# Optimization experiments

Measured on AMD Instinct MI355X. Metric: run time of the kernel, lower is better.

Reference implementation:

```python
import jax, jax.numpy as jnp
import numpy as np

B, S, HID = 2, 2048, 1024
H, KV, D = 8, 4, 128
GROUPS = H // KV
SCALE = D ** -0.5
ROPE_THETA = 10000.0


def _rope_tables(seq_len, dim):
    inv = 1.0 / (ROPE_THETA ** (jnp.arange(0, dim, 2, dtype=jnp.float32) / dim))
    t = jnp.arange(seq_len, dtype=jnp.float32)
    freqs = jnp.outer(t, inv)                          # [S, D/2]
    emb = jnp.concatenate([freqs, freqs], axis=-1)     # [S, D]
    return jnp.cos(emb), jnp.sin(emb)


def _rotate_half(x):
    x1, x2 = jnp.split(x, 2, axis=-1)
    return jnp.concatenate([-x2, x1], axis=-1)


def setup_inputs() -> dict:
    key = jax.random.key(0)
    ks = jax.random.split(key, 7)
    std = 0.02
    hidden = jax.random.normal(ks[0], (B, S, HID), jnp.float32)
    Wq = jax.random.normal(ks[1], (HID, H * D), jnp.float32) * std
    Wk = jax.random.normal(ks[2], (HID, KV * D), jnp.float32) * std
    Wv = jax.random.normal(ks[3], (HID, KV * D), jnp.float32) * std
    Wdt = jax.random.normal(ks[4], (KV * D, H), jnp.float32) * std
    A = jax.random.normal(ks[5], (H,), jnp.float32) * 0.1
    Wo = jax.random.normal(ks[6], (H * D, HID), jnp.float32) * std
    cos, sin = _rope_tables(S, D)
    causal_mask = jnp.triu(jnp.ones((S, S), jnp.int32), 1)[None, None]  # 1 = masked
    return dict(hidden=hidden, Wq=Wq, Wk=Wk, Wv=Wv, Wdt=Wdt, A=A, Wo=Wo,
                cos=cos, sin=sin, causal_mask=causal_mask)


def reference(hidden, Wq, Wk, Wv, Wdt, A, Wo, cos, sin, causal_mask):
    # q/k/v projections -> [B, heads, S, D]
    q = (hidden @ Wq).reshape(B, S, H, D).transpose(0, 2, 1, 3)
    k = (hidden @ Wk).reshape(B, S, KV, D).transpose(0, 2, 1, 3)
    v = (hidden @ Wv).reshape(B, S, KV, D).transpose(0, 2, 1, 3)
    # RoPE
    c = cos[None, None]  # [1,1,S,D]
    s = sin[None, None]
    q = q * c + _rotate_half(q) * s
    k = k * c + _rotate_half(k) * s
    # dynamic mask: dt_proj over flattened per-position value states
    v_flat = v.transpose(0, 2, 1, 3).reshape(B, S, KV * D)
    dt = v_flat @ Wdt                                        # [B, S, H]
    dyn = jnp.exp(A[None, None, :] * jax.nn.softplus(dt))    # [B, S, H]
    attn_bias = dyn.transpose(0, 2, 1)[:, :, None, :]        # [B, H, 1, kv]
    min_val = jnp.finfo(jnp.float32).min
    attn_bias = jnp.where(causal_mask != 0, min_val, attn_bias)  # [B, H, S, S]
    # GQA repeat of kv heads
    k_rep = jnp.repeat(k, GROUPS, axis=1)
    v_rep = jnp.repeat(v, GROUPS, axis=1)
    scores = jnp.einsum('bhqd,bhkd->bhqk', q, k_rep) * SCALE + attn_bias
    w = jax.nn.softmax(scores.astype(jnp.float32), axis=-1).astype(hidden.dtype)
    out = jnp.einsum('bhqk,bhkd->bhqd', w, v_rep)
    out = out.transpose(0, 2, 1, 3).reshape(B, S, H * D)
    return out @ Wo
```

## Files before the change

kernel.cpp:

```cpp
#include <hip/hip_runtime.h>

typedef unsigned short u16;
typedef unsigned int   u32;
typedef __bf16 bf16;
typedef bf16  bf16x8 __attribute__((ext_vector_type(8)));
typedef float f32x4  __attribute__((ext_vector_type(4)));

#define S_LEN 2048
#define SCALE 0.08838834764831845f
#define SMAX  8.0f

__device__ __forceinline__ float bf2f(u16 u) {
  union { u32 i; float f; } v; v.i = ((u32)u) << 16; return v.f;
}
__device__ __forceinline__ u16 f2b(float f) {
  union { float f; u32 i; } v; v.f = f;
  u32 x = v.i;
  u32 r = x + 0x7fffu + ((x >> 16) & 1u);
  return (u16)(r >> 16);
}
__device__ __forceinline__ float2 bfpair(u32 u) {
  union { u32 i; float f; } lo, hi;
  lo.i = u << 16; hi.i = u & 0xffff0000u;
  float2 r; r.x = lo.f; r.y = hi.f; return r;
}

__device__ __forceinline__ void gl_lds16(const u16* g, u16* l) {
  __builtin_amdgcn_global_load_lds(
      (const __attribute__((address_space(1))) void*)g,
      (__attribute__((address_space(3))) void*)l, 16, 0, 0);
}

__device__ __forceinline__ void load16(const float* p, u16* dst) {
  #pragma unroll
  for (int i = 0; i < 16; i += 4) {
    float4 v = *(const float4*)(p + i);
    dst[i]     = f2b(v.x); dst[i + 1] = f2b(v.y);
    dst[i + 2] = f2b(v.z); dst[i + 3] = f2b(v.w);
  }
}

__device__ __forceinline__ void storeo(float* p, float v) { *p = v; }
__device__ __forceinline__ void storeo(u16* p, float v)   { *p = f2b(v); }

__device__ __forceinline__ bf16x8 frag8(const u16* p) {
  union { uint4 u; bf16x8 v; } c;
  c.u = *(const uint4*)p;
  return c.v;
}
__device__ __forceinline__ f32x4 zero4() {
  f32x4 z = {0.f, 0.f, 0.f, 0.f}; return z;
}

__global__ __launch_bounds__(256) void prep_kernel(
    const float* __restrict__ H, u16* __restrict__ HB,
    const float* __restrict__ Wq, const float* __restrict__ Wk,
    const float* __restrict__ Wv, const float* __restrict__ Wo,
    u16* __restrict__ Wqt, u16* __restrict__ Wkt,
    u16* __restrict__ Wvt, u16* __restrict__ Wot)
{
  const int bid = blockIdx.x;
  if (bid < 2048) {
    const size_t base = ((size_t)bid * 256 + threadIdx.x) * 8;
    float4 a = *(const float4*)(H + base);
    float4 b = *(const float4*)(H + base + 4);
    u16 tmp[8];
    tmp[0]=f2b(a.x); tmp[1]=f2b(a.y); tmp[2]=f2b(a.z); tmp[3]=f2b(a.w);
    tmp[4]=f2b(b.x); tmp[5]=f2b(b.y); tmp[6]=f2b(b.z); tmp[7]=f2b(b.w);
    *(uint4*)(HB + base) = *(uint4*)tmp;
    return;
  }
  const int b2 = bid - 2048;
  const float* src; u16* dst; int N, ko, no;
  if (b2 < 256)      { src = Wq; dst = Wqt; N = 1024; int q = b2;       ko = (q >> 4) * 64; no = (q & 15) * 64; }
  else if (b2 < 384) { src = Wk; dst = Wkt; N = 512;  int q = b2 - 256; ko = (q >> 3) * 64; no = (q & 7) * 64; }
  else if (b2 < 512) { src = Wv; dst = Wvt; N = 512;  int q = b2 - 384; ko = (q >> 3) * 64; no = (q & 7) * 64; }
  else               { src = Wo; dst = Wot; N = 1024; int q = b2 - 512; ko = (q >> 4) * 64; no = (q & 15) * 64; }

  __shared__ __align__(16) u16 T[64][68];
  const int t = threadIdx.x;
  const int r = t >> 2, c = (t & 3) * 16;
  {
    u16 tmp[16];
    load16(src + (size_t)(ko + r) * N + no + c, tmp);
    *(uint4*)&T[r][c]     = *(uint4*)tmp;
    *(uint4*)&T[r][c + 8] = *(uint4*)(tmp + 8);
  }
  __syncthreads();
  {
    u16 tmp[16];
    #pragma unroll
    for (int j = 0; j < 16; ++j) tmp[j] = T[c + j][r];
    u16* o = dst + (size_t)(no + r) * 1024 + ko + c;
    *(uint4*)o       = *(uint4*)tmp;
    *(uint4*)(o + 8) = *(uint4*)(tmp + 8);
  }
}

__global__ __launch_bounds__(512) void gemm3(
    const u16* __restrict__ A, int lda, int Kdim,
    const u16* __restrict__ W0, u16* __restrict__ O0, int ldo0,
    const u16* __restrict__ W1, u16* __restrict__ O1, int ldo1,
    const u16* __restrict__ W2, u16* __restrict__ O2, int ldo2,
    int c1, int c2,
    const float* __restrict__ cosb, const float* __restrict__ sinb, int ropeLim,
    u16* __restrict__ VTg)
{
  const int flat = blockIdx.y * gridDim.x + blockIdx.x;
  const int xcd = flat & 7, rr = flat >> 3;
  const int bx = ((xcd & 1) << 3) + (rr & 7);
  const int by = ((xcd >> 1) << 3) + (rr >> 3);
  const int n0 = bx * 128;
  const int m0 = by * 128;
  const u16* W; u16* O; int ldo, col;
  if (n0 < c1)      { W = W0; O = O0; ldo = ldo0; col = n0; }
  else if (n0 < c2) { W = W1; O = O1; ldo = ldo1; col = n0 - c1; }
  else              { W = W2; O = O2; ldo = ldo2; col = n0 - c2; }
  const bool doRope = (n0 < ropeLim);
  const bool isV    = (n0 >= c2);

  __shared__ __align__(16) u16 As[2][128 * 64];
  __shared__ __align__(16) u16 Bs[2][128 * 64];

  const int t    = threadIdx.x;
  const int w    = t >> 6, lane = t & 63, quad = lane >> 4, l16 = lane & 15;
  const int sw   = l16 & 7;
  const int srow = lane >> 3;
  const int schk = (lane & 7) ^ srow;
  int kcs[2];
  #pragma unroll
  for (int ks = 0; ks < 2; ++ks) kcs[ks] = ((ks * 4 + quad) ^ sw) * 8;

  const u16* Ag = A + (size_t)(m0 + w * 16 + srow) * lda + schk * 8;
  const u16* Bg = W + (size_t)(col + w * 16 + srow) * Kdim + schk * 8;

  f32x4 acc[8];
  #pragma unroll
  for (int nt = 0; nt < 8; ++nt) acc[nt] = zero4();

  #pragma unroll
  for (int j = 0; j < 2; ++j) {
    gl_lds16(Ag + (size_t)(j * 8) * lda, &As[0][(w * 2 + j) * 512]);
    gl_lds16(Bg + (size_t)(j * 8) * Kdim, &Bs[0][(w * 2 + j) * 512]);
  }

  int cur = 0;
  for (int k0 = 0; k0 < Kdim; k0 += 64, cur ^= 1) {
    __syncthreads();
    if (k0 + 64 < Kdim) {
      #pragma unroll
      for (int j = 0; j < 2; ++j) {
        gl_lds16(Ag + (size_t)(j * 8) * lda + k0 + 64, &As[cur ^ 1][(w * 2 + j) * 512]);
        gl_lds16(Bg + (size_t)(j * 8) * Kdim + k0 + 64, &Bs[cur ^ 1][(w * 2 + j) * 512]);
      }
    }
    #pragma unroll
    for (int ks = 0; ks < 2; ++ks) {
      bf16x8 a0 = frag8(&As[cur][(w * 16 + l16) * 64 + kcs[ks]]);
      #pragma unroll
      for (int nt = 0; nt < 8; ++nt) {
        bf16x8 bw = frag8(&Bs[cur][(nt * 16 + l16) * 64 + kcs[ks]]);
        acc[nt] = __builtin_amdgcn_mfma_f32_16x16x32_bf16(a0, bw, acc[nt], 0, 0, 0);
      }
    }
  }

  if (doRope) {
    #pragma unroll
    for (int r = 0; r < 4; ++r) {
      const int m = m0 + w * 16 + quad * 4 + r;
      const int sp_ = m & (S_LEN - 1);
      const float* cp = cosb + (size_t)sp_ * 128;
      const float* sp = sinb + (size_t)sp_ * 128;
      #pragma unroll
      for (int nt = 0; nt < 4; ++nt) {
        const int d = nt * 16 + l16;
        const float a  = acc[nt][r];
        const float bb = acc[nt + 4][r];
        acc[nt][r]     = a * cp[d]       - bb * sp[d];
        acc[nt + 4][r] = bb * cp[d + 64] + a * sp[d + 64];
      }
    }
  }

  #pragma unroll
  for (int nt = 0; nt < 8; ++nt)
    #pragma unroll
    for (int r = 0; r < 4; ++r) {
      const int m = m0 + w * 16 + quad * 4 + r;
      const int n = col + nt * 16 + l16;
      O[(size_t)m * ldo + n] = f2b(acc[nt][r]);
    }

  if (isV) {
    #pragma unroll
    for (int nt = 0; nt < 8; ++nt) {
      const int m = m0 + w * 16 + quad * 4;
      const int bb_ = m >> 11, ss = m & (S_LEN - 1);
      const int d = col + nt * 16 + l16;
      u16 tmp4[4];
      #pragma unroll
      for (int r = 0; r < 4; ++r) tmp4[r] = f2b(acc[nt][r]);
      u16* dst = VTg + ((size_t)((bb_ * 4 + (d >> 7)) * 128 + (d & 127))) * S_LEN + ss;
      *(uint2*)dst = *(const uint2*)tmp4;
    }
  }
}

template <typename TO>
__global__ __launch_bounds__(512) void gemm2(
    const u16* __restrict__ A, int lda, int Kdim,
    const u16* __restrict__ W0, TO* __restrict__ O0, int ldo0,
    const u16* __restrict__ W1, TO* __restrict__ O1, int ldo1,
    const u16* __restrict__ W2, TO* __restrict__ O2, int ldo2,
    int c1, int c2)
{
  const int flat = blockIdx.y * gridDim.x + blockIdx.x;
  const int xcd = flat & 7, rr = flat >> 3;
  const int bx = ((xcd & 1) << 3) + (rr & 7);
  const int by = ((xcd >> 1) << 3) + (rr >> 3);
  const int n0 = bx * 64;
  const int m0 = by * 128;
  const u16* W; TO* O; int ldo, col;
  if (n0 < c1)      { W = W0; O = O0; ldo = ldo0; col = n0; }
  else if (n0 < c2) { W = W1; O = O1; ldo = ldo1; col = n0 - c1; }
  else              { W = W2; O = O2; ldo = ldo2; col = n0 - c2; }

  __shared__ __align__(16) u16 As[2][128 * 64];
  __shared__ __align__(16) u16 Bs[2][64 * 64];

  const int t    = threadIdx.x;
  const int w    = t >> 6, lane = t & 63, quad = lane >> 4, l16 = lane & 15;
  const int sw   = l16 & 7;
  const int srow = lane >> 3;
  const int schk = (lane & 7) ^ srow;
  int kcs[2];
  #pragma unroll
  for (int ks = 0; ks < 2; ++ks) kcs[ks] = ((ks * 4 + quad) ^ sw) * 8;

  const u16* Ag = A + (size_t)(m0 + w * 16 + srow) * lda + schk * 8;
  const u16* Bg = W + (size_t)(col + w * 8 + srow) * Kdim + schk * 8;

  f32x4 acc[4];
  #pragma unroll
  for (int nt = 0; nt < 4; ++nt) acc[nt] = zero4();

  #pragma unroll
  for (int j = 0; j < 2; ++j)
    gl_lds16(Ag + (size_t)(j * 8) * lda, &As[0][(w * 2 + j) * 512]);
  gl_lds16(Bg, &Bs[0][w * 512]);

  int cur = 0;
  for (int k0 = 0; k0 < Kdim; k0 += 64, cur ^= 1) {
    __syncthreads();
    if (k0 + 64 < Kdim) {
      #pragma unroll
      for (int j = 0; j < 2; ++j)
        gl_lds16(Ag + (size_t)(j * 8) * lda + k0 + 64, &As[cur ^ 1][(w * 2 + j) * 512]);
      gl_lds16(Bg + (size_t)k0 + 64, &Bs[cur ^ 1][w * 512]);
    }
    #pragma unroll
    for (int ks = 0; ks < 2; ++ks) {
      bf16x8 a0 = frag8(&As[cur][(w * 16 + l16) * 64 + kcs[ks]]);
      #pragma unroll
      for (int nt = 0; nt < 4; ++nt) {
        bf16x8 bw = frag8(&Bs[cur][(nt * 16 + l16) * 64 + kcs[ks]]);
        acc[nt] = __builtin_amdgcn_mfma_f32_16x16x32_bf16(a0, bw, acc[nt], 0, 0, 0);
      }
    }
  }
  #pragma unroll
  for (int nt = 0; nt < 4; ++nt)
    #pragma unroll
    for (int r = 0; r < 4; ++r) {
      const int m = m0 + w * 16 + quad * 4 + r;
      const int n = col + nt * 16 + l16;
      storeo(O + (size_t)m * ldo + n, acc[nt][r]);
    }
}

__global__ __launch_bounds__(256) void dyn_kernel(const u16* __restrict__ Vb, const float* __restrict__ Wdt,
                                                  const float* __restrict__ Af, float* __restrict__ dynT)
{
  __shared__ __align__(16) float Wl[4096];
  const int t = threadIdx.x;
  #pragma unroll
  for (int i = 0; i < 4; ++i)
    *(float4*)&Wl[(t + i * 256) * 4] = *(const float4*)(Wdt + (t + i * 256) * 4);
  __syncthreads();

  const int wid = t >> 6, lane = t & 63;
  const int pos = blockIdx.x * 4 + wid;
  float acc[8];
  #pragma unroll
  for (int h = 0; h < 8; ++h) acc[h] = 0.f;
  for (int j = lane; j < 512; j += 64) {
    float v = bf2f(Vb[(size_t)pos * 512 + j]);
    float4 w0 = *(const float4*)&Wl[j * 8];
    float4 w1 = *(const float4*)&Wl[j * 8 + 4];
    acc[0] += v * w0.x; acc[1] += v * w0.y; acc[2] += v * w0.z; acc[3] += v * w0.w;
    acc[4] += v * w1.x; acc[5] += v * w1.y; acc[6] += v * w1.z; acc[7] += v * w1.w;
  }
  #pragma unroll
  for (int off = 32; off > 0; off >>= 1)
    #pragma unroll
    for (int h = 0; h < 8; ++h) acc[h] += __shfl_down(acc[h], off, 64);
  if (lane == 0) {
    const int b = pos >> 11, s = pos & (S_LEN - 1);
    #pragma unroll
    for (int h = 0; h < 8; ++h) {
      float dt = acc[h];
      float sp = (dt > 20.f) ? dt : log1pf(__expf(dt));
      dynT[(size_t)(b * 8 + h) * S_LEN + s] = __expf(Af[h] * sp);
    }
  }
}

__global__ __launch_bounds__(256, 2) void attn_mfma(const u16* __restrict__ Qb, const u16* __restrict__ Kb,
                                                    const u16* __restrict__ VTg, const float* __restrict__ dynT,
                                                    u16* __restrict__ ctx,
                                                    u16* __restrict__ PO, float* __restrict__ PL)
{
  const int idx = blockIdx.x;
  const int g = (idx & 7) | (((idx >> 3) & 1) << 3);
  const int b = g >> 3, h = g & 7, kvh = h >> 1;
  const int f = idx >> 4;
  int s, c, kt0, kt1;
  if (f < 16)      { s = 16 + f; c = 0; kt0 = 0; kt1 = 7; }
  else if (f < 32) { s = 47 - f; c = 1; kt0 = 8; kt1 = s >> 1; }
  else             { s = 47 - f; c = 0; kt0 = 0; kt1 = s >> 1; }
  const int q0 = s * 64;
  const int dt = s >> 1;

  __shared__ __align__(16) u16 Ks[128 * 128];
  __shared__ __align__(16) u16 Vs[128 * 128];
  __shared__ __align__(16) u16 Ps[4][16 * 128];

  const int t = threadIdx.x;
  const int wid = t >> 6, lane = t & 63, quad = lane >> 4, l16 = lane & 15;
  const int sw = l16 & 7, hi = l16 >> 3;

  int kcs[4];
  #pragma unroll
  for (int ks = 0; ks < 4; ++ks) kcs[ks] = ((ks * 4 + quad) ^ sw) * 8;

  const u16* KgL[2];
  const u16* VgL[2];
  {
    const int g0 = hi * 8 + (sw ^ quad);
    const int g1 = hi * 8 + (sw ^ quad ^ 4);
    KgL[0] = Kb + (size_t)(b * S_LEN + wid * 32 + quad) * 512 + kvh * 128 + g0 * 8;
    KgL[1] = Kb + (size_t)(b * S_LEN + wid * 32 + 4 + quad) * 512 + kvh * 128 + g1 * 8;
    VgL[0] = VTg + ((size_t)((b * 4 + kvh) * 128 + wid * 32 + quad)) * S_LEN + g0 * 8;
    VgL[1] = VTg + ((size_t)((b * 4 + kvh) * 128 + wid * 32 + 4 + quad)) * S_LEN + g1 * 8;
  }

  bf16x8 qf[4];
  {
    const u16* qrow = Qb + (size_t)(b * S_LEN + q0 + wid * 16 + l16) * 1024 + h * 128 + quad * 8;
    #pragma unroll
    for (int ks = 0; ks < 4; ++ks) qf[ks] = frag8(qrow + ks * 32);
  }

  const float* dynbase = dynT + (size_t)(b * 8 + h) * S_LEN + l16;

  f32x4 accO[8];
  #pragma unroll
  for (int nt = 0; nt < 8; ++nt) accO[nt] = zero4();
  float l_lane[4] = {0.f, 0.f, 0.f, 0.f};

  for (int kt = kt0; kt <= kt1; ++kt) {
    const int k0 = kt * 128;
    __syncthreads();
    #pragma unroll
    for (int j = 0; j < 8; ++j)
      gl_lds16(KgL[j & 1] + (size_t)(k0 + (j >> 1) * 8) * 512, &Ks[(wid * 8 + j) * 512]);
    #pragma unroll
    for (int j = 0; j < 8; ++j)
      gl_lds16(VgL[j & 1] + (size_t)((j >> 1) * 8) * S_LEN + k0, &Vs[(wid * 8 + j) * 512]);
    float dv[8];
    #pragma unroll
    for (int nt = 0; nt < 8; ++nt) dv[nt] = dynbase[k0 + nt * 16];
    __syncthreads();

    f32x4 accS[8];
    #pragma unroll
    for (int nt = 0; nt < 8; ++nt) accS[nt] = zero4();
    __builtin_amdgcn_s_setprio(1);
    #pragma unroll
    for (int ks = 0; ks < 4; ++ks)
      #pragma unroll
      for (int nt = 0; nt < 8; ++nt)
        accS[nt] = __builtin_amdgcn_mfma_f32_16x16x32_bf16(
            qf[ks], frag8(&Ks[(nt * 16 + l16) * 128 + kcs[ks]]), accS[nt], 0, 0, 0);
    __builtin_amdgcn_s_setprio(0);

    if (kt < dt) {
      #pragma unroll
      for (int nt = 0; nt < 8; ++nt)
        #pragma unroll
        for (int r = 0; r < 4; ++r) {
          float p = __expf(fmaf(accS[nt][r], SCALE, dv[nt]) - SMAX);
          l_lane[r] += p;
          const int prow = quad * 4 + r;
          Ps[wid][prow * 128 + (((nt * 2 + hi) ^ (prow & 7)) << 3) + sw] = f2b(p);
        }
    } else {
      const int qq = (s & 1) * 64 + wid * 16 + quad * 4;
      #pragma unroll
      for (int nt = 0; nt < 8; ++nt) {
        const int kk = nt * 16 + l16;
        #pragma unroll
        for (int r = 0; r < 4; ++r) {
          float p = (kk > qq + r) ? 0.f
                    : __expf(fmaf(accS[nt][r], SCALE, dv[nt]) - SMAX);
          l_lane[r] += p;
          const int prow = quad * 4 + r;
          Ps[wid][prow * 128 + (((nt * 2 + hi) ^ (prow & 7)) << 3) + sw] = f2b(p);
        }
      }
    }

    __builtin_amdgcn_s_setprio(1);
    #pragma unroll
    for (int ks = 0; ks < 4; ++ks) {
      bf16x8 a = frag8(&Ps[wid][l16 * 128 + kcs[ks]]);
      #pragma unroll
      for (int nt = 0; nt < 8; ++nt)
        accO[nt] = __builtin_amdgcn_mfma_f32_16x16x32_bf16(
            a, frag8(&Vs[(nt * 16 + l16) * 128 + kcs[ks]]), accO[nt], 0, 0, 0);
    }
    __builtin_amdgcn_s_setprio(0);
  }

  #pragma unroll
  for (int off = 1; off < 16; off <<= 1)
    #pragma unroll
    for (int r = 0; r < 4; ++r) l_lane[r] += __shfl_xor(l_lane[r], off, 64);

  if (s < 16) {
    float linv[4];
    #pragma unroll
    for (int r = 0; r < 4; ++r) linv[r] = 1.f / l_lane[r];
    #pragma unroll
    for (int nt = 0; nt < 8; ++nt)
      #pragma unroll
      for (int r = 0; r < 4; ++r) {
        const int qq = q0 + wid * 16 + quad * 4 + r;
        const int d  = nt * 16 + l16;
        ctx[(size_t)(b * S_LEN + qq) * 1024 + h * 128 + d] = f2b(accO[nt][r] * linv[r]);
      }
  } else {
    const int slot = g * 32 + (s - 16) * 2 + c;
    u16 tmp[32];
    #pragma unroll
    for (int nt = 0; nt < 8; ++nt)
      #pragma unroll
      for (int r = 0; r < 4; ++r) tmp[nt * 4 + r] = f2b(accO[nt][r]);
    u16* po = PO + (size_t)slot * 8192 + wid * 2048 + lane * 32;
    #pragma unroll
    for (int i = 0; i < 4; ++i) *(uint4*)(po + i * 8) = *(uint4*)(tmp + i * 8);
    if (l16 == 0) {
      #pragma unroll
      for (int r = 0; r < 4; ++r) PL[slot * 64 + wid * 16 + quad * 4 + r] = l_lane[r];
    }
  }
}

__global__ __launch_bounds__(256) void attn_combine(const u16* __restrict__ PO, const float* __restrict__ PL,
                                                    u16* __restrict__ ctx)
{
  const int sx = (int)blockIdx.x;
  const int s = 16 + sx;
  const int g = (int)blockIdx.y;
  const int b = g >> 3, h = g & 7;
  const int slot0 = g * 32 + sx * 2;
  const int t = threadIdx.x;
  const int wid = t >> 6, lane = t & 63, quad = lane >> 4, l16 = lane & 15;

  float acc[32];
  #pragma unroll
  for (int i = 0; i < 32; ++i) acc[i] = 0.f;
  float ls[4] = {0.f, 0.f, 0.f, 0.f};

  #pragma unroll
  for (int cth = 0; cth < 2; ++cth) {
    const u16* po = PO + (size_t)(slot0 + cth) * 8192 + wid * 2048 + lane * 32;
    #pragma unroll
    for (int i = 0; i < 4; ++i) {
      uint4 v = *(const uint4*)(po + i * 8);
      u32 u[4] = {v.x, v.y, v.z, v.w};
      #pragma unroll
      for (int j = 0; j < 4; ++j) {
        float2 p = bfpair(u[j]);
        acc[i * 8 + 2 * j]     += p.x;
        acc[i * 8 + 2 * j + 1] += p.y;
      }
    }
    #pragma unroll
    for (int r = 0; r < 4; ++r) ls[r] += PL[(slot0 + cth) * 64 + wid * 16 + quad * 4 + r];
  }

  float linv[4];
  #pragma unroll
  for (int r = 0; r < 4; ++r) linv[r] = 1.f / ls[r];
  #pragma unroll
  for (int nt = 0; nt < 8; ++nt)
    #pragma unroll
    for (int r = 0; r < 4; ++r) {
      const int qq = s * 64 + wid * 16 + quad * 4 + r;
      const int d  = nt * 16 + l16;
      ctx[(size_t)(b * S_LEN + qq) * 1024 + h * 128 + d] = f2b(acc[nt * 4 + r] * linv[r]);
    }
}

extern "C" void kernel_launch(void* const* d_in, const int* in_sizes, int n_in,
                              void* d_out, int out_size, void* d_ws, size_t ws_size,
                              hipStream_t stream)
{
  const float* hidden = (const float*)d_in[0];
  const float* Wq     = (const float*)d_in[1];
  const float* Wk     = (const float*)d_in[2];
  const float* Wv     = (const float*)d_in[3];
  const float* Wdt    = (const float*)d_in[4];
  const float* Af     = (const float*)d_in[5];
  const float* Wo     = (const float*)d_in[6];
  const float* cosb   = (const float*)d_in[7];
  const float* sinb   = (const float*)d_in[8];
  float* out = (float*)d_out;

  u16* Qb  = (u16*)d_ws;
  u16* Kb  = Qb + (size_t)4096 * 1024;
  u16* Vb  = Kb + (size_t)4096 * 512;
  u16* VTg = Vb + (size_t)4096 * 512;
  float* dynT = (float*)(VTg + (size_t)4096 * 512);
  u16* PO = (u16*)(dynT + (size_t)16 * S_LEN);
  float* PL = (float*)(PO + (size_t)16 * 32 * 8192);
  u16* HB  = (u16*)(PL + (size_t)16 * 32 * 64);
  u16* Wqt = HB  + (size_t)4096 * 1024;
  u16* Wkt = Wqt + (size_t)1024 * 1024;
  u16* Wvt = Wkt + (size_t)512 * 1024;
  u16* Wot = Wvt + (size_t)512 * 1024;
  u16* ctx = Qb;

  prep_kernel<<<2816, 256, 0, stream>>>(hidden, HB, Wq, Wk, Wv, Wo, Wqt, Wkt, Wvt, Wot);
  gemm3<<<dim3(16, 32), 512, 0, stream>>>(HB, 1024, 1024,
      Wqt, Qb, 1024,
      Wkt, Kb,  512,
      Wvt, Vb,  512,
      1024, 1536,
      cosb, sinb, 1536, VTg);
  dyn_kernel<<<1024, 256, 0, stream>>>(Vb, Wdt, Af, dynT);
  attn_mfma<<<768, 256, 0, stream>>>(Qb, Kb, VTg, dynT, ctx, PO, PL);
  attn_combine<<<dim3(16, 16), 256, 0, stream>>>(PO, PL, ctx);
  gemm2<float><<<dim3(16, 32), 512, 0, stream>>>(ctx, 1024, 1024,
      Wot, out, 1024,
      Wot, out, 1024,
      Wot, out, 1024,
      1 << 30, 1 << 30);
}
```

Measured before the change: 196.1 us.

## Enlarge attention query tile to 128 rows with 8-wave blocks

The attention kernel now processes 128 query rows per block using 8 waves (512 threads) instead of 64 rows with 4 waves. Each K/V tile loaded into LDS is shared by twice as many query rows, which halves global K/V traffic per query. The causal split schedule and combine kernel are remapped to 128-row tiles with half as many blocks and partial slots. In exchange, there are fewer blocks in flight, the causal diagonal work is coarser, and larger LDS use per block may lower occupancy.

```diff
diff --git a/kernel.cpp b/kernel.cpp
--- a/kernel.cpp
+++ b/kernel.cpp
@@ -316,25 +316,27 @@
   }
 }
 
-__global__ __launch_bounds__(256, 2) void attn_mfma(const u16* __restrict__ Qb, const u16* __restrict__ Kb,
-                                                    const u16* __restrict__ VTg, const float* __restrict__ dynT,
-                                                    u16* __restrict__ ctx,
-                                                    u16* __restrict__ PO, float* __restrict__ PL)
+__global__ __launch_bounds__(512) void attn_mfma(const u16* __restrict__ Qb, const u16* __restrict__ Kb,
+                                                 const u16* __restrict__ VTg, const float* __restrict__ dynT,
+                                                 u16* __restrict__ ctx,
+                                                 u16* __restrict__ PO, float* __restrict__ PL)
 {
   const int idx = blockIdx.x;
   const int g = (idx & 7) | (((idx >> 3) & 1) << 3);
   const int b = g >> 3, h = g & 7, kvh = h >> 1;
   const int f = idx >> 4;
   int s, c, kt0, kt1;
-  if (f < 16)      { s = 16 + f; c = 0; kt0 = 0; kt1 = 7; }
-  else if (f < 32) { s = 47 - f; c = 1; kt0 = 8; kt1 = s >> 1; }
-  else             { s = 47 - f; c = 0; kt0 = 0; kt1 = s >> 1; }
-  const int q0 = s * 64;
-  const int dt = s >> 1;
+  if (f < 8) { s = 8 + f; c = 0; kt0 = 0; kt1 = 7; }
+  else {
+    const int j = (f - 8) >> 1;
+    if ((f & 1) == 0) { s = 7 - j;  c = 0; kt0 = 0; kt1 = s; }
+    else              { s = 15 - j; c = 1; kt0 = 8; kt1 = s; }
+  }
+  const int q0 = s * 128;
 
   __shared__ __align__(16) u16 Ks[128 * 128];
   __shared__ __align__(16) u16 Vs[128 * 128];
-  __shared__ __align__(16) u16 Ps[4][16 * 128];
+  __shared__ __align__(16) u16 Ps[8][16 * 128];
 
   const int t = threadIdx.x;
   const int wid = t >> 6, lane = t & 63, quad = lane >> 4, l16 = lane & 15;
@@ -344,15 +346,14 @@
   #pragma unroll
   for (int ks = 0; ks < 4; ++ks) kcs[ks] = ((ks * 4 + quad) ^ sw) * 8;
 
-  const u16* KgL[2];
-  const u16* VgL[2];
-  {
-    const int g0 = hi * 8 + (sw ^ quad);
-    const int g1 = hi * 8 + (sw ^ quad ^ 4);
-    KgL[0] = Kb + (size_t)(b * S_LEN + wid * 32 + quad) * 512 + kvh * 128 + g0 * 8;
-    KgL[1] = Kb + (size_t)(b * S_LEN + wid * 32 + 4 + quad) * 512 + kvh * 128 + g1 * 8;
-    VgL[0] = VTg + ((size_t)((b * 4 + kvh) * 128 + wid * 32 + quad)) * S_LEN + g0 * 8;
-    VgL[1] = VTg + ((size_t)((b * 4 + kvh) * 128 + wid * 32 + 4 + quad)) * S_LEN + g1 * 8;
+  const u16* KgL[4];
+  const u16* VgL[4];
+  #pragma unroll
+  for (int j = 0; j < 4; ++j) {
+    const int rloc = j * 4 + (lane >> 4);
+    const int gg = (lane & 15) ^ (rloc & 7);
+    KgL[j] = Kb + (size_t)(b * S_LEN + wid * 16 + rloc) * 512 + kvh * 128 + gg * 8;
+    VgL[j] = VTg + ((size_t)((b * 4 + kvh) * 128 + wid * 16 + rloc)) * S_LEN + gg * 8;
   }
 
   bf16x8 qf[4];
@@ -373,11 +374,11 @@
     const int k0 = kt * 128;
     __syncthreads();
     #pragma unroll
-    for (int j = 0; j < 8; ++j)
-      gl_lds16(KgL[j & 1] + (size_t)(k0 + (j >> 1) * 8) * 512, &Ks[(wid * 8 + j) * 512]);
-    #pragma unroll
-    for (int j = 0; j < 8; ++j)
-      gl_lds16(VgL[j & 1] + (size_t)((j >> 1) * 8) * S_LEN + k0, &Vs[(wid * 8 + j) * 512]);
+    for (int j = 0; j < 4; ++j)
+      gl_lds16(KgL[j] + (size_t)k0 * 512, &Ks[(wid * 4 + j) * 512]);
+    #pragma unroll
+    for (int j = 0; j < 4; ++j)
+      gl_lds16(VgL[j] + k0, &Vs[(wid * 4 + j) * 512]);
     float dv[8];
     #pragma unroll
     for (int nt = 0; nt < 8; ++nt) dv[nt] = dynbase[k0 + nt * 16];
@@ -395,7 +396,7 @@
             qf[ks], frag8(&Ks[(nt * 16 + l16) * 128 + kcs[ks]]), accS[nt], 0, 0, 0);
     __builtin_amdgcn_s_setprio(0);
 
-    if (kt < dt) {
+    if (kt < s) {
       #pragma unroll
       for (int nt = 0; nt < 8; ++nt)
         #pragma unroll
@@ -406,7 +407,7 @@
           Ps[wid][prow * 128 + (((nt * 2 + hi) ^ (prow & 7)) << 3) + sw] = f2b(p);
         }
     } else {
-      const int qq = (s & 1) * 64 + wid * 16 + quad * 4;
+      const int qq = wid * 16 + quad * 4;
       #pragma unroll
       for (int nt = 0; nt < 8; ++nt) {
         const int kk = nt * 16 + l16;
@@ -438,7 +439,7 @@
     #pragma unroll
     for (int r = 0; r < 4; ++r) l_lane[r] += __shfl_xor(l_lane[r], off, 64);
 
-  if (s < 16) {
+  if (s < 8) {
     float linv[4];
     #pragma unroll
     for (int r = 0; r < 4; ++r) linv[r] = 1.f / l_lane[r];
@@ -451,30 +452,30 @@
         ctx[(size_t)(b * S_LEN + qq) * 1024 + h * 128 + d] = f2b(accO[nt][r] * linv[r]);
       }
   } else {
-    const int slot = g * 32 + (s - 16) * 2 + c;
+    const int slot = g * 16 + (s - 8) * 2 + c;
     u16 tmp[32];
     #pragma unroll
     for (int nt = 0; nt < 8; ++nt)
       #pragma unroll
       for (int r = 0; r < 4; ++r) tmp[nt * 4 + r] = f2b(accO[nt][r]);
-    u16* po = PO + (size_t)slot * 8192 + wid * 2048 + lane * 32;
+    u16* po = PO + (size_t)slot * 16384 + wid * 2048 + lane * 32;
     #pragma unroll
     for (int i = 0; i < 4; ++i) *(uint4*)(po + i * 8) = *(uint4*)(tmp + i * 8);
     if (l16 == 0) {
       #pragma unroll
-      for (int r = 0; r < 4; ++r) PL[slot * 64 + wid * 16 + quad * 4 + r] = l_lane[r];
-    }
-  }
-}
-
-__global__ __launch_bounds__(256) void attn_combine(const u16* __restrict__ PO, const float* __restrict__ PL,
+      for (int r = 0; r < 4; ++r) PL[slot * 128 + wid * 16 + quad * 4 + r] = l_lane[r];
+    }
+  }
+}
+
+__global__ __launch_bounds__(512) void attn_combine(const u16* __restrict__ PO, const float* __restrict__ PL,
                                                     u16* __restrict__ ctx)
 {
   const int sx = (int)blockIdx.x;
-  const int s = 16 + sx;
+  const int s = 8 + sx;
   const int g = (int)blockIdx.y;
   const int b = g >> 3, h = g & 7;
-  const int slot0 = g * 32 + sx * 2;
+  const int slot0 = g * 16 + sx * 2;
   const int t = threadIdx.x;
   const int wid = t >> 6, lane = t & 63, quad = lane >> 4, l16 = lane & 15;
 
@@ -485,7 +486,7 @@
 
   #pragma unroll
   for (int cth = 0; cth < 2; ++cth) {
-    const u16* po = PO + (size_t)(slot0 + cth) * 8192 + wid * 2048 + lane * 32;
+    const u16* po = PO + (size_t)(slot0 + cth) * 16384 + wid * 2048 + lane * 32;
     #pragma unroll
     for (int i = 0; i < 4; ++i) {
       uint4 v = *(const uint4*)(po + i * 8);
@@ -498,7 +499,7 @@
       }
     }
     #pragma unroll
-    for (int r = 0; r < 4; ++r) ls[r] += PL[(slot0 + cth) * 64 + wid * 16 + quad * 4 + r];
+    for (int r = 0; r < 4; ++r) ls[r] += PL[(slot0 + cth) * 128 + wid * 16 + quad * 4 + r];
   }
 
   float linv[4];
@@ -508,7 +509,7 @@
   for (int nt = 0; nt < 8; ++nt)
     #pragma unroll
     for (int r = 0; r < 4; ++r) {
-      const int qq = s * 64 + wid * 16 + quad * 4 + r;
+      const int qq = s * 128 + wid * 16 + quad * 4 + r;
       const int d  = nt * 16 + l16;
       ctx[(size_t)(b * S_LEN + qq) * 1024 + h * 128 + d] = f2b(acc[nt * 4 + r] * linv[r]);
     }
@@ -535,8 +536,8 @@
   u16* VTg = Vb + (size_t)4096 * 512;
   float* dynT = (float*)(VTg + (size_t)4096 * 512);
   u16* PO = (u16*)(dynT + (size_t)16 * S_LEN);
-  float* PL = (float*)(PO + (size_t)16 * 32 * 8192);
-  u16* HB  = (u16*)(PL + (size_t)16 * 32 * 64);
+  float* PL = (float*)(PO + (size_t)16 * 16 * 16384);
+  u16* HB  = (u16*)(PL + (size_t)16 * 16 * 128);
   u16* Wqt = HB  + (size_t)4096 * 1024;
   u16* Wkt = Wqt + (size_t)1024 * 1024;
   u16* Wvt = Wkt + (size_t)512 * 1024;
@@ -551,8 +552,8 @@
       1024, 1536,
       cosb, sinb, 1536, VTg);
   dyn_kernel<<<1024, 256, 0, stream>>>(Vb, Wdt, Af, dynT);
-  attn_mfma<<<768, 256, 0, stream>>>(Qb, Kb, VTg, dynT, ctx, PO, PL);
-  attn_combine<<<dim3(16, 16), 256, 0, stream>>>(PO, PL, ctx);
+  attn_mfma<<<384, 512, 0, stream>>>(Qb, Kb, VTg, dynT, ctx, PO, PL);
+  attn_combine<<<dim3(8, 16), 512, 0, stream>>>(PO, PL, ctx);
   gemm2<float><<<dim3(16, 32), 512, 0, stream>>>(ctx, 1024, 1024,
       Wot, out, 1024,
       Wot, out, 1024,
```

New measurement: 203.8 us. +3.9%, slower.

## Remove split-KV partial attention and combine kernel, use one block per query tile

Applied to the files above, without the earlier changes.

Drops the split-KV scheme, in which long query tiles were divided into two key-range chunks whose partial outputs were written to a workspace and merged by a separate combine kernel. Each block now processes one 64-row query tile over all its causal key tiles and normalizes and writes ctx directly. Tiles are ordered longest first, so the grid shrinks from 768 to 512 blocks. This removes the extra launch and the partial-output traffic, at the cost of worse load balance from long serial key loops on the last query tiles.

```diff
diff --git a/kernel.cpp b/kernel.cpp
--- a/kernel.cpp
+++ b/kernel.cpp
@@ -18,11 +18,6 @@
   u32 x = v.i;
   u32 r = x + 0x7fffu + ((x >> 16) & 1u);
   return (u16)(r >> 16);
-}
-__device__ __forceinline__ float2 bfpair(u32 u) {
-  union { u32 i; float f; } lo, hi;
-  lo.i = u << 16; hi.i = u & 0xffff0000u;
-  float2 r; r.x = lo.f; r.y = hi.f; return r;
 }
 
 __device__ __forceinline__ void gl_lds16(const u16* g, u16* l) {
@@ -318,17 +313,13 @@
 
 __global__ __launch_bounds__(256, 2) void attn_mfma(const u16* __restrict__ Qb, const u16* __restrict__ Kb,
                                                     const u16* __restrict__ VTg, const float* __restrict__ dynT,
-                                                    u16* __restrict__ ctx,
-                                                    u16* __restrict__ PO, float* __restrict__ PL)
+                                                    u16* __restrict__ ctx)
 {
   const int idx = blockIdx.x;
   const int g = (idx & 7) | (((idx >> 3) & 1) << 3);
   const int b = g >> 3, h = g & 7, kvh = h >> 1;
   const int f = idx >> 4;
-  int s, c, kt0, kt1;
-  if (f < 16)      { s = 16 + f; c = 0; kt0 = 0; kt1 = 7; }
-  else if (f < 32) { s = 47 - f; c = 1; kt0 = 8; kt1 = s >> 1; }
-  else             { s = 47 - f; c = 0; kt0 = 0; kt1 = s >> 1; }
+  const int s = (f < 16) ? (31 - f) : (f - 16);
   const int q0 = s * 64;
   const int dt = s >> 1;
 
@@ -369,7 +360,7 @@
   for (int nt = 0; nt < 8; ++nt) accO[nt] = zero4();
   float l_lane[4] = {0.f, 0.f, 0.f, 0.f};
 
-  for (int kt = kt0; kt <= kt1; ++kt) {
+  for (int kt = 0; kt <= dt; ++kt) {
     const int k0 = kt * 128;
     __syncthreads();
     #pragma unroll
@@ -438,79 +429,16 @@
     #pragma unroll
     for (int r = 0; r < 4; ++r) l_lane[r] += __shfl_xor(l_lane[r], off, 64);
 
-  if (s < 16) {
-    float linv[4];
-    #pragma unroll
-    for (int r = 0; r < 4; ++r) linv[r] = 1.f / l_lane[r];
-    #pragma unroll
-    for (int nt = 0; nt < 8; ++nt)
-      #pragma unroll
-      for (int r = 0; r < 4; ++r) {
-        const int qq = q0 + wid * 16 + quad * 4 + r;
-        const int d  = nt * 16 + l16;
-        ctx[(size_t)(b * S_LEN + qq) * 1024 + h * 128 + d] = f2b(accO[nt][r] * linv[r]);
-      }
-  } else {
-    const int slot = g * 32 + (s - 16) * 2 + c;
-    u16 tmp[32];
-    #pragma unroll
-    for (int nt = 0; nt < 8; ++nt)
-      #pragma unroll
-      for (int r = 0; r < 4; ++r) tmp[nt * 4 + r] = f2b(accO[nt][r]);
-    u16* po = PO + (size_t)slot * 8192 + wid * 2048 + lane * 32;
-    #pragma unroll
-    for (int i = 0; i < 4; ++i) *(uint4*)(po + i * 8) = *(uint4*)(tmp + i * 8);
-    if (l16 == 0) {
-      #pragma unroll
-      for (int r = 0; r < 4; ++r) PL[slot * 64 + wid * 16 + quad * 4 + r] = l_lane[r];
-    }
-  }
-}
-
-__global__ __launch_bounds__(256) void attn_combine(const u16* __restrict__ PO, const float* __restrict__ PL,
-                                                    u16* __restrict__ ctx)
-{
-  const int sx = (int)blockIdx.x;
-  const int s = 16 + sx;
-  const int g = (int)blockIdx.y;
-  const int b = g >> 3, h = g & 7;
-  const int slot0 = g * 32 + sx * 2;
-  const int t = threadIdx.x;
-  const int wid = t >> 6, lane = t & 63, quad = lane >> 4, l16 = lane & 15;
-
-  float acc[32];
-  #pragma unroll
-  for (int i = 0; i < 32; ++i) acc[i] = 0.f;
-  float ls[4] = {0.f, 0.f, 0.f, 0.f};
-
-  #pragma unroll
-  for (int cth = 0; cth < 2; ++cth) {
-    const u16* po = PO + (size_t)(slot0 + cth) * 8192 + wid * 2048 + lane * 32;
-    #pragma unroll
-    for (int i = 0; i < 4; ++i) {
-      uint4 v = *(const uint4*)(po + i * 8);
-      u32 u[4] = {v.x, v.y, v.z, v.w};
-      #pragma unroll
-      for (int j = 0; j < 4; ++j) {
-        float2 p = bfpair(u[j]);
-        acc[i * 8 + 2 * j]     += p.x;
-        acc[i * 8 + 2 * j + 1] += p.y;
-      }
-    }
-    #pragma unroll
-    for (int r = 0; r < 4; ++r) ls[r] += PL[(slot0 + cth) * 64 + wid * 16 + quad * 4 + r];
-  }
-
   float linv[4];
   #pragma unroll
-  for (int r = 0; r < 4; ++r) linv[r] = 1.f / ls[r];
+  for (int r = 0; r < 4; ++r) linv[r] = 1.f / l_lane[r];
   #pragma unroll
   for (int nt = 0; nt < 8; ++nt)
     #pragma unroll
     for (int r = 0; r < 4; ++r) {
-      const int qq = s * 64 + wid * 16 + quad * 4 + r;
+      const int qq = q0 + wid * 16 + quad * 4 + r;
       const int d  = nt * 16 + l16;
-      ctx[(size_t)(b * S_LEN + qq) * 1024 + h * 128 + d] = f2b(acc[nt * 4 + r] * linv[r]);
+      ctx[(size_t)(b * S_LEN + qq) * 1024 + h * 128 + d] = f2b(accO[nt][r] * linv[r]);
     }
 }
 
@@ -534,9 +462,7 @@
   u16* Vb  = Kb + (size_t)4096 * 512;
   u16* VTg = Vb + (size_t)4096 * 512;
   float* dynT = (float*)(VTg + (size_t)4096 * 512);
-  u16* PO = (u16*)(dynT + (size_t)16 * S_LEN);
-  float* PL = (float*)(PO + (size_t)16 * 32 * 8192);
-  u16* HB  = (u16*)(PL + (size_t)16 * 32 * 64);
+  u16* HB  = (u16*)(dynT + (size_t)16 * S_LEN);
   u16* Wqt = HB  + (size_t)4096 * 1024;
   u16* Wkt = Wqt + (size_t)1024 * 1024;
   u16* Wvt = Wkt + (size_t)512 * 1024;
@@ -551,8 +477,7 @@
       1024, 1536,
       cosb, sinb, 1536, VTg);
   dyn_kernel<<<1024, 256, 0, stream>>>(Vb, Wdt, Af, dynT);
-  attn_mfma<<<768, 256, 0, stream>>>(Qb, Kb, VTg, dynT, ctx, PO, PL);
-  attn_combine<<<dim3(16, 16), 256, 0, stream>>>(PO, PL, ctx);
+  attn_mfma<<<512, 256, 0, stream>>>(Qb, Kb, VTg, dynT, ctx);
   gemm2<float><<<dim3(16, 32), 512, 0, stream>>>(ctx, 1024, 1024,
       Wot, out, 1024,
       Wot, out, 1024,
```

After: 201.1 us. +2.5%, slower.
